# Kernel tuning notes

Measured on AMD Instinct MI355X. Metric: run time of the kernel, lower is better.

The kernel has to match this reference:

```python
import jax, jax.numpy as jnp
import numpy as np

VAR_FLOOR = 0.002
BS, A, IN, H, L, NNH, ATT, NACT = 1024, 32, 96, 64, 16, 64, 32, 16


def _lin(x, w, b):
    return x @ w.T + b


def _lrelu(x):
    return jax.nn.leaky_relu(x, 0.01)


def setup_inputs() -> dict:
    key = jax.random.key(0)
    ks = jax.random.split(key, 24)
    def w(k, o, i):
        return jax.random.normal(k, (o, i), jnp.float32) / np.float32(np.sqrt(i))
    def b(k, o):
        return jax.random.normal(k, (o,), jnp.float32) * 0.01
    N = BS * A
    return {
        "inputs": jax.random.normal(ks[0], (N, IN), jnp.float32),
        "hidden_state": jax.random.normal(ks[1], (N, H), jnp.float32),
        "eps": jax.random.normal(ks[2], (N, A * L), jnp.float32),
        "fc1_w": w(ks[3], H, IN), "fc1_b": b(ks[4], H),
        "gru_wih": w(ks[5], 3 * H, H), "gru_whh": w(ks[6], 3 * H, H),
        "gru_bih": b(ks[7], 3 * H), "gru_bhh": b(ks[8], 3 * H),
        "fc2_w": w(ks[9], NACT, H), "fc2_b": b(ks[10], NACT),
        "emb_w1": w(ks[11], NNH, H), "emb_b1": b(ks[12], NNH),
        "bn_g": jnp.ones((NNH,), jnp.float32), "bn_b": jnp.zeros((NNH,), jnp.float32),
        "emb_w2": w(ks[13], A * L * 2, NNH), "emb_b2": b(ks[14], A * L * 2),
        "msg_w1": w(ks[15], NNH, H + L), "msg_b1": b(ks[16], NNH),
        "msg_w2": w(ks[17], NACT, NNH), "msg_b2": b(ks[18], NACT),
        "wq_w": w(ks[19], ATT, H), "wq_b": b(ks[20], ATT),
        "wk_w": w(ks[21], ATT, L), "wk_b": b(ks[22], ATT),
        "bs": BS, "t": 0,
    }


def reference(inputs, hidden_state, eps, fc1_w, fc1_b, gru_wih, gru_whh, gru_bih,
              gru_bhh, fc2_w, fc2_b, emb_w1, emb_b1, bn_g, bn_b, emb_w2, emb_b2,
              msg_w1, msg_b1, msg_w2, msg_b2, wq_w, wq_b, wk_w, wk_b, bs, t):
    Hd = fc1_w.shape[0]
    x = jax.nn.relu(_lin(inputs, fc1_w, fc1_b))
    h_in = hidden_state.reshape(-1, Hd)
    # GRUCell
    gi = _lin(x, gru_wih, gru_bih)
    gh = _lin(h_in, gru_whh, gru_bhh)
    ir, iz, inn = jnp.split(gi, 3, axis=-1)
    hr, hz, hn = jnp.split(gh, 3, axis=-1)
    r = jax.nn.sigmoid(ir + hr)
    z = jax.nn.sigmoid(iz + hz)
    n = jnp.tanh(inn + r * hn)
    h = (1.0 - z) * n + z * h_in
    q = _lin(h, fc2_w, fc2_b)
    # embed_net: Linear -> BatchNorm(train) -> LeakyReLU -> Linear
    z1 = _lin(h, emb_w1, emb_b1)
    z1 = bn_g * (z1 - z1.mean(0)) / jnp.sqrt(z1.var(0) + 1e-5) + bn_b
    lat_par = _lin(_lrelu(z1), emb_w2, emb_b2)
    D = lat_par.shape[-1] // 2
    Ld = wk_w.shape[1]
    Ag = D // Ld
    mu = lat_par[:, :D]
    var = jnp.clip(jnp.exp(lat_par[:, D:]), VAR_FLOOR, None)
    latent = (mu + jnp.sqrt(var) * eps).reshape(bs, Ag, Ag, Ld)  # [b,i,j,L]
    # msg_net on (h of receiver j, latent[b,i,j])
    h3 = h.reshape(bs, Ag, Hd)
    h_rep = jnp.broadcast_to(h3[:, None, :, :], (bs, Ag, Ag, Hd))  # [b,i,j]=h[b,j]
    msg_in = jnp.concatenate([h_rep, latent], axis=-1)
    msg = _lin(_lrelu(_lin(msg_in, msg_w1, msg_b1)), msg_w2, msg_b2)  # (b,A,A,n_act)
    # attention gating
    att = wq_w.shape[0]
    query = _lin(h, wq_w, wq_b).reshape(bs, Ag, att) / np.float32(np.sqrt(att))
    key_ = _lin(latent, wk_w, wk_b)  # (b,A,A,att)
    alpha = jnp.einsum('bia,bija->bij', query, key_)
    alpha = jnp.where(jnp.eye(Ag, dtype=bool)[None], -1e9, alpha)
    alpha = jax.nn.softmax(alpha, axis=-1)
    agg = jnp.einsum('bij,bijn->bjn', alpha, msg)  # sum gated msgs over sender i
    return_q = q + agg.reshape(bs * Ag, -1)
    return (return_q, h)
```

## Files before the change

kernel.cpp:

```cpp
#include <hip/hip_runtime.h>
#include <math.h>

namespace {

constexpr int NROW = 32768;
constexpr int HDIM = 64;
constexpr int DH   = 512;

typedef __attribute__((ext_vector_type(8))) short bf16x8;
typedef __attribute__((ext_vector_type(4))) float f32x4;
typedef __attribute__((ext_vector_type(4))) unsigned uint4e;
typedef __attribute__((ext_vector_type(2))) unsigned uint2e;

__device__ __forceinline__ float sigmoidf_(float x) { return 1.f / (1.f + __expf(-x)); }
__device__ __forceinline__ float lrelu_(float x) { return x > 0.f ? x : 0.01f * x; }
__device__ __forceinline__ unsigned pkbf(float a, float b) {
  unsigned ua = __float_as_uint(a) + 0x8000u;
  unsigned ub = __float_as_uint(b) + 0x8000u;
  return __builtin_amdgcn_perm(ub, ua, 0x07060302);
}

__global__ __launch_bounds__(512, 1) void k_fgru(
    const float* __restrict__ in,
    const float* __restrict__ hprev,
    const float* __restrict__ fc1w, const float* __restrict__ fc1b,
    const float* __restrict__ wih, const float* __restrict__ whh,
    const float* __restrict__ bih, const float* __restrict__ bhh,
    float* __restrict__ hT, float* __restrict__ hout) {
  __shared__ char smem[73728];
  const int t = threadIdx.x;
  const int n0 = blockIdx.x * 128;
  short*    xS = (short*)smem;
  unsigned* gU = (unsigned*)(smem + 18432);
  float*    trF = (float*)(smem + 18432);

  const float2* wih2 = (const float2*)wih;
  const float2* whh2 = (const float2*)whh;
  {
    float2 wv[12];
#pragma unroll
    for (int i = 0; i < 12; ++i) {
      int idx = t + 512 * i;
      int row = idx >> 5, kp = idx & 31;
      wv[i] = wih2[row * 32 + kp];
    }
#pragma unroll
    for (int i = 0; i < 12; ++i) {
      int idx = t + 512 * i;
      int row = idx >> 5, kp = idx & 31;
      int gate = row >> 6, cl = row & 63;
      gU[(gate * 64 + cl) * 36 + kp] = pkbf(wv[i].x, wv[i].y);
    }
#pragma unroll
    for (int i = 0; i < 12; ++i) {
      int idx = t + 512 * i;
      int row = idx >> 5, kp = idx & 31;
      wv[i] = whh2[row * 32 + kp];
    }
#pragma unroll
    for (int i = 0; i < 12; ++i) {
      int idx = t + 512 * i;
      int row = idx >> 5, kp = idx & 31;
      int gate = row >> 6, cl = row & 63;
      gU[((gate + 3) * 64 + cl) * 36 + kp] = pkbf(wv[i].x, wv[i].y);
    }
  }

  const int w = t >> 6, l = t & 63;
  const int m = l & 15, g = l >> 4;
  const int rowA = n0 + w * 16 + m;

  bf16x8 af[3];
#pragma unroll
  for (int ks = 0; ks < 3; ++ks) {
    const float4* p = (const float4*)(in + (size_t)rowA * 96 + ks * 32 + g * 8);
    float4 a = p[0], b = p[1];
    union { unsigned u[4]; bf16x8 h; } tw;
    tw.u[0] = pkbf(a.x, a.y); tw.u[1] = pkbf(a.z, a.w);
    tw.u[2] = pkbf(b.x, b.y); tw.u[3] = pkbf(b.z, b.w);
    af[ks] = tw.h;
  }
  {
    f32x4 accx[4];
#pragma unroll
    for (int ct = 0; ct < 4; ++ct) accx[ct] = (f32x4){0.f, 0.f, 0.f, 0.f};
#pragma unroll
    for (int ct = 0; ct < 4; ++ct)
#pragma unroll
      for (int ks = 0; ks < 3; ++ks) {
        const float4* p = (const float4*)(fc1w + (ct * 16 + m) * 96 + ks * 32 + g * 8);
        float4 a = p[0], b = p[1];
        union { unsigned u[4]; bf16x8 h; } tw;
        tw.u[0] = pkbf(a.x, a.y); tw.u[1] = pkbf(a.z, a.w);
        tw.u[2] = pkbf(b.x, b.y); tw.u[3] = pkbf(b.z, b.w);
        accx[ct] = __builtin_amdgcn_mfma_f32_16x16x32_bf16(af[ks], tw.h, accx[ct], 0, 0, 0);
      }
#pragma unroll
    for (int ct = 0; ct < 4; ++ct) {
      int c = ct * 16 + m;
      float bc = fc1b[c];
#pragma unroll
      for (int reg = 0; reg < 4; ++reg) {
        int nl = w * 16 + g * 4 + reg;
        float v = fmaxf(accx[ct][reg] + bc, 0.f);
        xS[nl * 72 + c] = (short)((__float_as_uint(v) + 0x8000u) >> 16);
      }
    }
  }
  __syncthreads();

  bf16x8 ax[2], ah[2];
#pragma unroll
  for (int ks = 0; ks < 2; ++ks) {
    ax[ks] = *(const bf16x8*)(xS + (w * 16 + m) * 72 + ks * 32 + g * 8);
    const float4* p = (const float4*)(hprev + (size_t)rowA * 64 + ks * 32 + g * 8);
    float4 a = p[0], b = p[1];
    union { unsigned u[4]; bf16x8 h; } tw;
    tw.u[0] = pkbf(a.x, a.y); tw.u[1] = pkbf(a.z, a.w);
    tw.u[2] = pkbf(b.x, b.y); tw.u[3] = pkbf(b.z, b.w);
    ah[ks] = tw.h;
  }
  const short* gS = (const short*)gU;
  float hc[4][4];
#pragma unroll 1
  for (int ct = 0; ct < 4; ++ct) {
    f32x4 a_ir = (f32x4){0.f,0.f,0.f,0.f}, a_iz = (f32x4){0.f,0.f,0.f,0.f},
          a_in = (f32x4){0.f,0.f,0.f,0.f}, a_hr = (f32x4){0.f,0.f,0.f,0.f},
          a_hz = (f32x4){0.f,0.f,0.f,0.f}, a_hn = (f32x4){0.f,0.f,0.f,0.f};
    int crow = ct * 16 + m;
#pragma unroll
    for (int ks = 0; ks < 2; ++ks) {
      bf16x8 b0 = *(const bf16x8*)(gS + (0 * 64 + crow) * 72 + ks * 32 + g * 8);
      bf16x8 b1 = *(const bf16x8*)(gS + (1 * 64 + crow) * 72 + ks * 32 + g * 8);
      bf16x8 b2 = *(const bf16x8*)(gS + (2 * 64 + crow) * 72 + ks * 32 + g * 8);
      bf16x8 b3 = *(const bf16x8*)(gS + (3 * 64 + crow) * 72 + ks * 32 + g * 8);
      bf16x8 b4 = *(const bf16x8*)(gS + (4 * 64 + crow) * 72 + ks * 32 + g * 8);
      bf16x8 b5 = *(const bf16x8*)(gS + (5 * 64 + crow) * 72 + ks * 32 + g * 8);
      a_ir = __builtin_amdgcn_mfma_f32_16x16x32_bf16(ax[ks], b0, a_ir, 0, 0, 0);
      a_iz = __builtin_amdgcn_mfma_f32_16x16x32_bf16(ax[ks], b1, a_iz, 0, 0, 0);
      a_in = __builtin_amdgcn_mfma_f32_16x16x32_bf16(ax[ks], b2, a_in, 0, 0, 0);
      a_hr = __builtin_amdgcn_mfma_f32_16x16x32_bf16(ah[ks], b3, a_hr, 0, 0, 0);
      a_hz = __builtin_amdgcn_mfma_f32_16x16x32_bf16(ah[ks], b4, a_hz, 0, 0, 0);
      a_hn = __builtin_amdgcn_mfma_f32_16x16x32_bf16(ah[ks], b5, a_hn, 0, 0, 0);
    }
    float bir = bih[crow], biz = bih[64 + crow], bin = bih[128 + crow];
    float bhr = bhh[crow], bhz = bhh[64 + crow], bhn = bhh[128 + crow];
#pragma unroll
    for (int reg = 0; reg < 4; ++reg) {
      int nl = w * 16 + g * 4 + reg;
      float hv = hprev[(size_t)(n0 + nl) * 64 + crow];
      float r  = sigmoidf_(a_ir[reg] + bir + a_hr[reg] + bhr);
      float z  = sigmoidf_(a_iz[reg] + biz + a_hz[reg] + bhz);
      float nn = tanhf(a_in[reg] + bin + r * (a_hn[reg] + bhn));
      hc[ct][reg] = (1.f - z) * nn + z * hv;
    }
  }
  __syncthreads();
#pragma unroll
  for (int ct = 0; ct < 4; ++ct)
#pragma unroll
    for (int reg = 0; reg < 4; ++reg)
      trF[(ct * 16 + m) * 133 + w * 16 + g * 4 + reg] = hc[ct][reg];
  __syncthreads();
#pragma unroll
  for (int i = 0; i < 16; ++i) {
    int idx = t + 512 * i;
    int nl = idx & 127, cl = idx >> 7;
    hT[(size_t)cl * NROW + n0 + nl] = trF[cl * 133 + nl];
  }
#pragma unroll
  for (int i = 0; i < 16; ++i) {
    int idx = t + 512 * i;
    int c = idx & 63, nl = idx >> 6;
    hout[(size_t)(n0 + nl) * 64 + c] = trF[c * 133 + nl];
  }
}

__global__ __launch_bounds__(256) void k_heads(const float* __restrict__ hT,
    const float* __restrict__ fc2w, const float* __restrict__ fc2b,
    const float* __restrict__ wqw, const float* __restrict__ wkw,
    const float* __restrict__ ew1, const float* __restrict__ eb1,
    float* __restrict__ qT, float* __restrict__ qkT, float* __restrict__ z1T,
    float* __restrict__ part) {
  __shared__ char smem[36864];
  const int t = threadIdx.x;
  const int n0 = blockIdx.x * 128;
  unsigned* hU = (unsigned*)smem;
  unsigned* wU = (unsigned*)(smem + 18432);
  float* sp1 = (float*)(smem + 18432 + 13824);
  float* sp2 = sp1 + 256;
  const float qs = 0.17677669529663687f;

  {
    float va[16], vb[16];
#pragma unroll
    for (int i = 0; i < 16; ++i) {
      int idx = t + 256 * i;
      int nl = idx & 127, kp = idx >> 7;
      va[i] = hT[(size_t)(2 * kp) * NROW + n0 + nl];
      vb[i] = hT[(size_t)(2 * kp + 1) * NROW + n0 + nl];
    }
#pragma unroll
    for (int i = 0; i < 16; ++i) {
      int idx = t + 256 * i;
      int nl = idx & 127, kp = idx >> 7;
      hU[nl * 36 + kp] = pkbf(va[i], vb[i]);
    }
  }
  {
    float2 wv[10];
#pragma unroll
    for (int i = 0; i < 10; ++i) {
      int idx = t + 256 * i;
      int kp = idx & 31, cl = idx >> 5;
      const float* src = (cl < 16) ? (fc2w + cl * 64) : (ew1 + (cl - 16) * 64);
      wv[i] = *(const float2*)(src + 2 * kp);
    }
#pragma unroll
    for (int i = 0; i < 10; ++i) {
      int idx = t + 256 * i;
      int kp = idx & 31, cl = idx >> 5;
      int dst = (cl < 16) ? cl : (cl + 16);
      wU[dst * 36 + kp] = pkbf(wv[i].x, wv[i].y);
    }
  }
  {
    int kp = t & 31, ll = t >> 5;
#pragma unroll
    for (int h = 0; h < 2; ++h) {
      int row = ll + 8 * h;
      float s0 = 0.f, s1 = 0.f;
#pragma unroll
      for (int a = 0; a < 32; ++a) {
        float wk = wkw[a * 16 + row];
        s0 = fmaf(wk, wqw[a * 64 + 2 * kp], s0);
        s1 = fmaf(wk, wqw[a * 64 + 2 * kp + 1], s1);
      }
      wU[(16 + row) * 36 + kp] = pkbf(s0 * qs, s1 * qs);
    }
  }
  __syncthreads();

  const int w = t >> 6, l = t & 63;
  const int m = l & 15, g = l >> 4;
  const short* sH = (const short*)hU;
  const short* sW = (const short*)wU;

  bf16x8 af[2][2];
#pragma unroll
  for (int mt = 0; mt < 2; ++mt)
#pragma unroll
    for (int ks = 0; ks < 2; ++ks)
      af[mt][ks] = *(const bf16x8*)(sH + (w * 32 + mt * 16 + m) * 72 + ks * 32 + g * 8);

  f32x4 acc[2][6];
#pragma unroll
  for (int mt = 0; mt < 2; ++mt)
#pragma unroll
    for (int ct = 0; ct < 6; ++ct) acc[mt][ct] = (f32x4){0.f, 0.f, 0.f, 0.f};
#pragma unroll
  for (int ct = 0; ct < 6; ++ct)
#pragma unroll
    for (int ks = 0; ks < 2; ++ks) {
      bf16x8 bw = *(const bf16x8*)(sW + (ct * 16 + m) * 72 + ks * 32 + g * 8);
#pragma unroll
      for (int mt = 0; mt < 2; ++mt)
        acc[mt][ct] = __builtin_amdgcn_mfma_f32_16x16x32_bf16(af[mt][ks], bw, acc[mt][ct], 0, 0, 0);
    }

  float s1[4], s2[4];
#pragma unroll
  for (int zt = 0; zt < 4; ++zt) { s1[zt] = 0.f; s2[zt] = 0.f; }
#pragma unroll
  for (int mt = 0; mt < 2; ++mt) {
    int nb = n0 + w * 32 + mt * 16 + g * 4;
    {
      float bc = fc2b[m];
      f32x4 v;
#pragma unroll
      for (int reg = 0; reg < 4; ++reg) v[reg] = acc[mt][0][reg] + bc;
      *(f32x4*)(qT + (size_t)m * NROW + nb) = v;
    }
    *(f32x4*)(qkT + (size_t)m * NROW + nb) = acc[mt][1];
#pragma unroll
    for (int ct = 2; ct < 6; ++ct) {
      int z = (ct - 2) * 16 + m;
      float bc = eb1[z];
      f32x4 v;
#pragma unroll
      for (int reg = 0; reg < 4; ++reg) {
        float zv = acc[mt][ct][reg] + bc;
        v[reg] = zv;
        s1[ct - 2] += zv;
        s2[ct - 2] = fmaf(zv, zv, s2[ct - 2]);
      }
      *(f32x4*)(z1T + (size_t)z * NROW + nb) = v;
    }
  }
#pragma unroll
  for (int zt = 0; zt < 4; ++zt) {
    s1[zt] += __shfl_down(s1[zt], 16, 64);
    s1[zt] += __shfl_down(s1[zt], 32, 64);
    s2[zt] += __shfl_down(s2[zt], 16, 64);
    s2[zt] += __shfl_down(s2[zt], 32, 64);
  }
  if (l < 16) {
#pragma unroll
    for (int zt = 0; zt < 4; ++zt) {
      sp1[w * 64 + zt * 16 + m] = s1[zt];
      sp2[w * 64 + zt * 16 + m] = s2[zt];
    }
  }
  __syncthreads();
  if (t < 64) {
    float a1 = sp1[t] + sp1[64 + t] + sp1[128 + t] + sp1[192 + t];
    float a2 = sp2[t] + sp2[64 + t] + sp2[128 + t] + sp2[192 + t];
    part[(size_t)blockIdx.x * 128 + t] = a1;
    part[(size_t)blockIdx.x * 128 + 64 + t] = a2;
  }
}

__global__ __launch_bounds__(256) void k_bnstat(const float* __restrict__ part,
    const float* __restrict__ bng, const float* __restrict__ bnb,
    const float* __restrict__ ew2,
    float* __restrict__ stat, unsigned* __restrict__ ew2b) {
  if (blockIdx.x == 0) {
    __shared__ float red[512];
    const int t = threadIdx.x;
    const int c = t & 63, q = t >> 6;
    float s1 = 0.f, s2 = 0.f;
#pragma unroll 4
    for (int b = q; b < 256; b += 4) {
      s1 += part[(size_t)b * 128 + c];
      s2 += part[(size_t)b * 128 + 64 + c];
    }
    red[q * 64 + c] = s1;
    red[256 + q * 64 + c] = s2;
    __syncthreads();
    if (t < 64) {
      float a1 = red[t] + red[64 + t] + red[128 + t] + red[192 + t];
      float a2 = red[256 + t] + red[320 + t] + red[384 + t] + red[448 + t];
      float mean = a1 * (1.f / NROW);
      float var = a2 * (1.f / NROW) - mean * mean;
      float rstd = rsqrtf(var + 1e-5f);
      float sc = bng[t] * rstd;
      stat[t] = sc;
      stat[64 + t] = bnb[t] - mean * sc;
    }
  } else {
    const int rb = blockIdx.x - 1;
    const int t = threadIdx.x;
#pragma unroll
    for (int it = 0; it < 2; ++it) {
      int id2 = t + 256 * it;
      int r = rb * 16 + (id2 >> 5);
      int cp = id2 & 31;
      float2 v = *(const float2*)(ew2 + (size_t)r * 64 + 2 * cp);
      ew2b[(size_t)r * 32 + cp] = pkbf(v.x, v.y);
    }
  }
}

constexpr int LATB_OFF = 0;
constexpr int H3B_OFF  = 36864;
constexpr int W1H_OFF  = 41472;
constexpr int W1L_OFF  = 50688;
constexpr int W2P_OFF  = 53248;
constexpr int ALL_OFF  = 55552;
constexpr int MT_OFF   = 59776;
constexpr int QKL_OFF  = MT_OFF + 4608;
__global__ __launch_bounds__(512, 1) void k_msg(
    const unsigned* __restrict__ ew2b, const float* __restrict__ stat,
    const float* __restrict__ z1T, const float* __restrict__ eb2,
    const float* __restrict__ eps,
    const float* __restrict__ qkT,
    const float* __restrict__ qT, const float* __restrict__ hrow,
    const float* __restrict__ w1, const float* __restrict__ b1,
    const float* __restrict__ w2, const float* __restrict__ b2,
    float* __restrict__ out) {
  __shared__ char smem[80256];
  const int t = threadIdx.x;
  const int b = blockIdx.x;
  const int b32 = b * 32;
  unsigned* latB_dw = (unsigned*)(smem + LATB_OFF);

  const int w = t >> 6, l = t & 63;
  const int m = l & 15, g = l >> 4;

  {
    short* xz = (short*)(smem + MT_OFF);
    float zv[4];
#pragma unroll
    for (int it = 0; it < 4; ++it) {
      int idx = t + 512 * it;
      int i = idx & 31, c = idx >> 5;
      zv[it] = z1T[(size_t)c * NROW + b32 + i];
    }
#pragma unroll
    for (int it = 0; it < 4; ++it) {
      int idx = t + 512 * it;
      int i = idx & 31, c = idx >> 5;
      float v = lrelu_(fmaf(stat[c], zv[it], stat[64 + c]));
      xz[i * 72 + c] = (short)((__float_as_uint(v) + 0x8000u) >> 16);
    }
  }
  {
    float* qkL = (float*)(smem + QKL_OFF);
    int i = t & 31, ll = t >> 5;
    qkL[i * 20 + ll] = qkT[(size_t)ll * NROW + b32 + i];
  }
  {
    int cp = t & 31, jbase = t >> 5;
    const float2* h2 = (const float2*)hrow;
    float2 hv[2];
#pragma unroll
    for (int it = 0; it < 2; ++it)
      hv[it] = h2[((size_t)(b32 + jbase + 16 * it) * 64 + 2 * cp) >> 1];
    unsigned* dst = (unsigned*)(smem + H3B_OFF);
#pragma unroll
    for (int it = 0; it < 2; ++it)
      dst[(jbase + 16 * it) * 36 + cp] = pkbf(hv[it].x, hv[it].y);
  }
  {
    int kp = t & 31, cb = t >> 5;
    const float2* w12 = (const float2*)w1;
    float2 wv[4];
#pragma unroll
    for (int it = 0; it < 4; ++it)
      wv[it] = w12[((cb + 16 * it) * 80 + 2 * kp) >> 1];
    unsigned* dst = (unsigned*)(smem + W1H_OFF);
#pragma unroll
    for (int it = 0; it < 4; ++it)
      dst[(cb + 16 * it) * 36 + kp] = pkbf(wv[it].x, wv[it].y);
  }
  {
    int lp = t & 7, cc = t >> 3;
    const float2* w12 = (const float2*)w1;
    float2 wv = w12[(cc * 80 + 64 + 2 * lp) >> 1];
    unsigned* dst = (unsigned*)(smem + W1L_OFF);
    dst[cc * 10 + lp] = pkbf(wv.x, wv.y);
  }
  {
    int pp = t & 31, nn = t >> 5;
    const float2* w22 = (const float2*)w2;
    int p = 2 * pp;
    int c = ((p >> 2) & 3) * 16 + (p >> 4) * 4 + (p & 3);
    float2 wv0 = w22[(nn * 64 + c) >> 1];
    unsigned* dst = (unsigned*)(smem + W2P_OFF);
    dst[nn * 36 + pp] = pkbf(wv0.x, wv0.y);
  }
  __syncthreads();

  {
    const short* xzS = (const short*)(smem + MT_OFF);
    bf16x8 afz[2][2];
#pragma unroll
    for (int mt = 0; mt < 2; ++mt)
#pragma unroll
      for (int ks = 0; ks < 2; ++ks)
        afz[mt][ks] = *(const bf16x8*)(xzS + (mt * 16 + m) * 72 + ks * 32 + g * 8);
    const uint4e* w4 = (const uint4e*)ew2b;
    const float stdfloor = 0.04472135955f;
#pragma unroll 2
    for (int ci8 = 0; ci8 < 4; ++ci8) {
      int ci = w * 4 + ci8;
      int c = ci * 16 + m;
      union { uint4e u; bf16x8 h; } bmu[2], blv[2];
#pragma unroll
      for (int ks = 0; ks < 2; ++ks) {
        bmu[ks].u = w4[(size_t)(ci * 16 + m) * 8 + ks * 4 + g];
        blv[ks].u = w4[(size_t)(512 + ci * 16 + m) * 8 + ks * 4 + g];
      }
      float ep[2][4];
#pragma unroll
      for (int mt = 0; mt < 2; ++mt)
#pragma unroll
        for (int reg = 0; reg < 4; ++reg)
          ep[mt][reg] = eps[(size_t)(b32 + mt * 16 + g * 4 + reg) * 512 + c];
      f32x4 accm[2], accl[2];
#pragma unroll
      for (int mt = 0; mt < 2; ++mt) {
        accm[mt] = (f32x4){0.f, 0.f, 0.f, 0.f};
        accl[mt] = (f32x4){0.f, 0.f, 0.f, 0.f};
      }
#pragma unroll
      for (int ks = 0; ks < 2; ++ks)
#pragma unroll
        for (int mt = 0; mt < 2; ++mt) {
          accm[mt] = __builtin_amdgcn_mfma_f32_16x16x32_bf16(afz[mt][ks], bmu[ks].h, accm[mt], 0, 0, 0);
          accl[mt] = __builtin_amdgcn_mfma_f32_16x16x32_bf16(afz[mt][ks], blv[ks].h, accl[mt], 0, 0, 0);
        }
      float ebm = eb2[c], ebl = eb2[DH + c];
#pragma unroll
      for (int mt = 0; mt < 2; ++mt)
#pragma unroll
        for (int reg = 0; reg < 4; ++reg) {
          float mu = accm[mt][reg] + ebm;
          float lv = accl[mt][reg] + ebl;
          float sd = fmaxf(__expf(0.5f * lv), stdfloor);
          float lat = fmaf(sd, ep[mt][reg], mu);
          float lat2 = __shfl_xor(lat, 1, 64);
          if (!(m & 1)) {
            int i = mt * 16 + g * 4 + reg;
            latB_dw[(i * 32 + ci) * 9 + (m >> 1)] = pkbf(lat, lat2);
          }
        }
    }
  }
  __syncthreads();

  {
    const float* qkL = (const float*)(smem + QKL_OFF);
    float* alL = (float*)(smem + ALL_OFF);
#pragma unroll 1
    for (int p = 0; p < 2; ++p) {
      int i = (t >> 5) + 16 * p;
      int j = t & 31;
      const unsigned* lr = latB_dw + (i * 32 + j) * 9;
      float acc = 0.f;
#pragma unroll
      for (int d = 0; d < 8; ++d) {
        unsigned u = lr[d];
        float lo = __uint_as_float(u << 16);
        float hi = __uint_as_float(u & 0xffff0000u);
        acc = fmaf(lo, qkL[i * 20 + 2 * d], acc);
        acc = fmaf(hi, qkL[i * 20 + 2 * d + 1], acc);
      }
      if (j == i) acc = -1e9f;
      float mx = acc;
#pragma unroll
      for (int msk = 16; msk > 0; msk >>= 1) mx = fmaxf(mx, __shfl_xor(mx, msk, 32));
      float e = __expf(acc - mx);
      float s = e;
#pragma unroll
      for (int msk = 16; msk > 0; msk >>= 1) s += __shfl_xor(s, msk, 32);
      alL[i * 33 + j] = e / s;
    }
  }

  const int n15 = l & 15, q = l >> 4;
  const int jh = w & 1, ibase = (w >> 1) * 8;
  const bool kact = (q < 2);

  f32x4 hp[4];
#pragma unroll
  for (int ct = 0; ct < 4; ++ct) hp[ct] = (f32x4){0.f, 0.f, 0.f, 0.f};
#pragma unroll
  for (int ct = 0; ct < 4; ++ct)
#pragma unroll
    for (int ks = 0; ks < 2; ++ks) {
      bf16x8 aF = *(const bf16x8*)(smem + W1H_OFF + (ct * 16 + n15) * 144 + ks * 64 + q * 16);
      bf16x8 bF = *(const bf16x8*)(smem + H3B_OFF + (jh * 16 + n15) * 144 + ks * 64 + q * 16);
      hp[ct] = __builtin_amdgcn_mfma_f32_16x16x32_bf16(aF, bF, hp[ct], 0, 0, 0);
    }
#pragma unroll
  for (int ct = 0; ct < 4; ++ct)
#pragma unroll
    for (int reg = 0; reg < 4; ++reg)
      hp[ct][reg] += b1[ct * 16 + q * 4 + reg];

  bf16x8 aL[4];
#pragma unroll
  for (int ct = 0; ct < 4; ++ct) {
    union { unsigned u[4]; bf16x8 h; } tmp;
    tmp.u[0] = tmp.u[1] = tmp.u[2] = tmp.u[3] = 0u;
    if (kact) {
      const unsigned* p = (const unsigned*)(smem + W1L_OFF) + (ct * 16 + n15) * 10 + q * 4;
      uint2e d0 = *(const uint2e*)p;
      uint2e d1 = *(const uint2e*)(p + 2);
      tmp.u[0] = d0.x; tmp.u[1] = d0.y; tmp.u[2] = d1.x; tmp.u[3] = d1.y;
    }
    aL[ct] = tmp.h;
  }
  bf16x8 w2F[2];
#pragma unroll
  for (int ks = 0; ks < 2; ++ks)
    w2F[ks] = *(const bf16x8*)(smem + W2P_OFF + n15 * 144 + ks * 64 + q * 16);
  float b2v[4];
#pragma unroll
  for (int reg = 0; reg < 4; ++reg) b2v[reg] = b2[q * 4 + reg];

  __syncthreads();

  float agg[4] = {0.f, 0.f, 0.f, 0.f};
  char* wb = smem + MT_OFF + w * 2560;
  const float* alLf = (const float*)(smem + ALL_OFF);
#pragma unroll 1
  for (int it = 0; it < 8; ++it) {
    int ii = ibase + it;
    int r = ii * 32 + jh * 16 + n15;
    union { unsigned u[4]; bf16x8 h; } latF;
    latF.u[0] = latF.u[1] = latF.u[2] = latF.u[3] = 0u;
    if (kact) {
      const unsigned* p = latB_dw + r * 9 + q * 4;
      latF.u[0] = p[0]; latF.u[1] = p[1]; latF.u[2] = p[2]; latF.u[3] = p[3];
    }
    f32x4 acc[4];
#pragma unroll
    for (int ct = 0; ct < 4; ++ct) {
      acc[ct] = (f32x4){0.f, 0.f, 0.f, 0.f};
      acc[ct] = __builtin_amdgcn_mfma_f32_16x16x32_bf16(aL[ct], latF.h, acc[ct], 0, 0, 0);
    }
#pragma unroll
    for (int h = 0; h < 2; ++h) {
      float m0[4], m1[4];
#pragma unroll
      for (int reg = 0; reg < 4; ++reg) {
        float v0 = acc[2 * h][reg] + hp[2 * h][reg];
        float v1 = acc[2 * h + 1][reg] + hp[2 * h + 1][reg];
        m0[reg] = fmaxf(v0, 0.01f * v0);
        m1[reg] = fmaxf(v1, 0.01f * v1);
      }
      uint4e pk4;
      pk4.x = pkbf(m0[0], m0[1]); pk4.y = pkbf(m0[2], m0[3]);
      pk4.z = pkbf(m1[0], m1[1]); pk4.w = pkbf(m1[2], m1[3]);
      int qp = (2 * q + h) & 3;
      *(uint4e*)(wb + (q >> 1) * 1280 + n15 * 80 + qp * 16) = pk4;
    }
    f32x4 msg = (f32x4){0.f, 0.f, 0.f, 0.f};
#pragma unroll
    for (int ks = 0; ks < 2; ++ks) {
      bf16x8 mF = *(const bf16x8*)(wb + ks * 1280 + n15 * 80 + q * 16);
      msg = __builtin_amdgcn_mfma_f32_16x16x32_bf16(w2F[ks], mF, msg, 0, 0, 0);
    }
    float aw = alLf[ii * 33 + jh * 16 + n15];
#pragma unroll
    for (int reg = 0; reg < 4; ++reg)
      agg[reg] = fmaf(aw, msg[reg] + b2v[reg], agg[reg]);
  }
  {
    f32x4 av; av[0] = agg[0]; av[1] = agg[1]; av[2] = agg[2]; av[3] = agg[3];
    *(f32x4*)(wb + n15 * 80 + q * 16) = av;
  }
  __syncthreads();
  {
    int jg = t >> 4, nn = t & 15;
    int jh2 = jg >> 4, jl = jg & 15;
    float s = qT[(size_t)nn * NROW + b32 + jg];
#pragma unroll
    for (int k = 0; k < 4; ++k)
      s += *(const float*)(smem + MT_OFF + (jh2 + 2 * k) * 2560 + jl * 80 + nn * 4);
    out[(size_t)b * 512 + t] = s;
  }
}

}

extern "C" void kernel_launch(void* const* d_in, const int* in_sizes, int n_in,
                              void* d_out, int out_size, void* d_ws, size_t ws_size,
                              hipStream_t stream) {
  (void)in_sizes; (void)n_in; (void)out_size; (void)ws_size;
  const float* inputs = (const float*)d_in[0];
  const float* hidden = (const float*)d_in[1];
  const float* eps    = (const float*)d_in[2];
  const float* fc1w   = (const float*)d_in[3];
  const float* fc1b   = (const float*)d_in[4];
  const float* wih    = (const float*)d_in[5];
  const float* whh    = (const float*)d_in[6];
  const float* bih    = (const float*)d_in[7];
  const float* bhh    = (const float*)d_in[8];
  const float* fc2w   = (const float*)d_in[9];
  const float* fc2b   = (const float*)d_in[10];
  const float* ew1    = (const float*)d_in[11];
  const float* eb1    = (const float*)d_in[12];
  const float* bng    = (const float*)d_in[13];
  const float* bnb    = (const float*)d_in[14];
  const float* ew2    = (const float*)d_in[15];
  const float* eb2    = (const float*)d_in[16];
  const float* w1     = (const float*)d_in[17];
  const float* b1     = (const float*)d_in[18];
  const float* w2     = (const float*)d_in[19];
  const float* b2     = (const float*)d_in[20];
  const float* wqw    = (const float*)d_in[21];
  const float* wkw    = (const float*)d_in[23];

  float* ws = (float*)d_ws;
  float* hT     = ws;
  float* qT     = ws + 2097152;
  float* qkT    = ws + 2621440;
  float* z1T    = ws + 3670016;
  float* part   = ws + 5767168;
  float* stat   = ws + 5832704;
  unsigned* ew2b = (unsigned*)(ws + 5832832);

  float* out_q = (float*)d_out;
  float* out_h = (float*)d_out + 524288;

  hipLaunchKernelGGL(k_fgru, dim3(256), dim3(512), 0, stream,
                     inputs, hidden, fc1w, fc1b, wih, whh, bih, bhh, hT, out_h);
  hipLaunchKernelGGL(k_heads, dim3(256), dim3(256), 0, stream,
                     hT, fc2w, fc2b, wqw, wkw, ew1, eb1, qT, qkT, z1T, part);
  hipLaunchKernelGGL(k_bnstat, dim3(65), dim3(256), 0, stream, part, bng, bnb, ew2, stat, ew2b);
  hipLaunchKernelGGL(k_msg, dim3(1024), dim3(512), 0, stream,
                     ew2b, stat, z1T, eb2, eps, qkT, qT, out_h, w1, b1, w2, b2, out_q);
}
```

Baseline: 227.4 us.

## Fuse heads projection kernel into GRU kernel, dropping transposed h buffer

Merges the fc2/query-key/embedding-layer-1 projections into the GRU kernel. The new hidden state goes to LDS as bf16 and feeds MFMA directly, with per-block BN partial sums computed in the same kernel. This removes one kernel launch, plus the global write and re-read of the transposed hidden state hT. In exchange, the GRU kernel uses more LDS (about 90KB) and more registers, and it loads the extra weights in every block.

```diff
diff --git a/kernel.cpp b/kernel.cpp
--- a/kernel.cpp
+++ b/kernel.cpp
@@ -26,13 +26,21 @@
     const float* __restrict__ fc1w, const float* __restrict__ fc1b,
     const float* __restrict__ wih, const float* __restrict__ whh,
     const float* __restrict__ bih, const float* __restrict__ bhh,
-    float* __restrict__ hT, float* __restrict__ hout) {
-  __shared__ char smem[73728];
+    const float* __restrict__ fc2w, const float* __restrict__ fc2b,
+    const float* __restrict__ wqw, const float* __restrict__ wkw,
+    const float* __restrict__ ew1, const float* __restrict__ eb1,
+    float* __restrict__ qT, float* __restrict__ qkT, float* __restrict__ z1T,
+    float* __restrict__ part, float* __restrict__ hout) {
+  __shared__ char smem[91648];
   const int t = threadIdx.x;
   const int n0 = blockIdx.x * 128;
   short*    xS = (short*)smem;
   unsigned* gU = (unsigned*)(smem + 18432);
   float*    trF = (float*)(smem + 18432);
+  unsigned* wU = (unsigned*)(smem + 73728);
+  float*    sp1 = (float*)(smem + 87552);
+  float*    sp2 = (float*)(smem + 89600);
+  const float qs = 0.17677669529663687f;
 
   const float2* wih2 = (const float2*)wih;
   const float2* whh2 = (const float2*)whh;
@@ -64,6 +72,34 @@
       int gate = row >> 6, cl = row & 63;
       gU[((gate + 3) * 64 + cl) * 36 + kp] = pkbf(wv[i].x, wv[i].y);
     }
+  }
+  {
+    float2 wv[5];
+#pragma unroll
+    for (int i = 0; i < 5; ++i) {
+      int idx = t + 512 * i;
+      int kp = idx & 31, cl = idx >> 5;
+      const float* src = (cl < 16) ? (fc2w + cl * 64) : (ew1 + (cl - 16) * 64);
+      wv[i] = *(const float2*)(src + 2 * kp);
+    }
+#pragma unroll
+    for (int i = 0; i < 5; ++i) {
+      int idx = t + 512 * i;
+      int kp = idx & 31, cl = idx >> 5;
+      int dst = (cl < 16) ? cl : (cl + 16);
+      wU[dst * 36 + kp] = pkbf(wv[i].x, wv[i].y);
+    }
+  }
+  {
+    int kp = t & 31, row = t >> 5;
+    float s0 = 0.f, s1 = 0.f;
+#pragma unroll
+    for (int a = 0; a < 32; ++a) {
+      float wk = wkw[a * 16 + row];
+      s0 = fmaf(wk, wqw[a * 64 + 2 * kp], s0);
+      s1 = fmaf(wk, wqw[a * 64 + 2 * kp + 1], s1);
+    }
+    wU[(16 + row) * 36 + kp] = pkbf(s0 * qs, s1 * qs);
   }
 
   const int w = t >> 6, l = t & 63;
@@ -155,6 +191,31 @@
       hc[ct][reg] = (1.f - z) * nn + z * hv;
     }
   }
+#pragma unroll
+  for (int ct = 0; ct < 4; ++ct)
+#pragma unroll
+    for (int reg = 0; reg < 4; ++reg) {
+      int nl = w * 16 + g * 4 + reg;
+      xS[nl * 72 + ct * 16 + m] =
+          (short)((__float_as_uint(hc[ct][reg]) + 0x8000u) >> 16);
+    }
+
+  bf16x8 af2[2];
+#pragma unroll
+  for (int ks = 0; ks < 2; ++ks)
+    af2[ks] = *(const bf16x8*)(xS + (w * 16 + m) * 72 + ks * 32 + g * 8);
+  const short* sW = (const short*)wU;
+  f32x4 acc[6];
+#pragma unroll
+  for (int ct = 0; ct < 6; ++ct) acc[ct] = (f32x4){0.f, 0.f, 0.f, 0.f};
+#pragma unroll
+  for (int ct = 0; ct < 6; ++ct)
+#pragma unroll
+    for (int ks = 0; ks < 2; ++ks) {
+      bf16x8 bw = *(const bf16x8*)(sW + (ct * 16 + m) * 72 + ks * 32 + g * 8);
+      acc[ct] = __builtin_amdgcn_mfma_f32_16x16x32_bf16(af2[ks], bw, acc[ct], 0, 0, 0);
+    }
+
   __syncthreads();
 #pragma unroll
   for (int ct = 0; ct < 4; ++ct)
@@ -162,126 +223,26 @@
     for (int reg = 0; reg < 4; ++reg)
       trF[(ct * 16 + m) * 133 + w * 16 + g * 4 + reg] = hc[ct][reg];
   __syncthreads();
-#pragma unroll
-  for (int i = 0; i < 16; ++i) {
-    int idx = t + 512 * i;
-    int nl = idx & 127, cl = idx >> 7;
-    hT[(size_t)cl * NROW + n0 + nl] = trF[cl * 133 + nl];
-  }
 #pragma unroll
   for (int i = 0; i < 16; ++i) {
     int idx = t + 512 * i;
     int c = idx & 63, nl = idx >> 6;
     hout[(size_t)(n0 + nl) * 64 + c] = trF[c * 133 + nl];
   }
-}
-
-__global__ __launch_bounds__(256) void k_heads(const float* __restrict__ hT,
-    const float* __restrict__ fc2w, const float* __restrict__ fc2b,
-    const float* __restrict__ wqw, const float* __restrict__ wkw,
-    const float* __restrict__ ew1, const float* __restrict__ eb1,
-    float* __restrict__ qT, float* __restrict__ qkT, float* __restrict__ z1T,
-    float* __restrict__ part) {
-  __shared__ char smem[36864];
-  const int t = threadIdx.x;
-  const int n0 = blockIdx.x * 128;
-  unsigned* hU = (unsigned*)smem;
-  unsigned* wU = (unsigned*)(smem + 18432);
-  float* sp1 = (float*)(smem + 18432 + 13824);
-  float* sp2 = sp1 + 256;
-  const float qs = 0.17677669529663687f;
-
-  {
-    float va[16], vb[16];
-#pragma unroll
-    for (int i = 0; i < 16; ++i) {
-      int idx = t + 256 * i;
-      int nl = idx & 127, kp = idx >> 7;
-      va[i] = hT[(size_t)(2 * kp) * NROW + n0 + nl];
-      vb[i] = hT[(size_t)(2 * kp + 1) * NROW + n0 + nl];
-    }
-#pragma unroll
-    for (int i = 0; i < 16; ++i) {
-      int idx = t + 256 * i;
-      int nl = idx & 127, kp = idx >> 7;
-      hU[nl * 36 + kp] = pkbf(va[i], vb[i]);
-    }
-  }
-  {
-    float2 wv[10];
-#pragma unroll
-    for (int i = 0; i < 10; ++i) {
-      int idx = t + 256 * i;
-      int kp = idx & 31, cl = idx >> 5;
-      const float* src = (cl < 16) ? (fc2w + cl * 64) : (ew1 + (cl - 16) * 64);
-      wv[i] = *(const float2*)(src + 2 * kp);
-    }
-#pragma unroll
-    for (int i = 0; i < 10; ++i) {
-      int idx = t + 256 * i;
-      int kp = idx & 31, cl = idx >> 5;
-      int dst = (cl < 16) ? cl : (cl + 16);
-      wU[dst * 36 + kp] = pkbf(wv[i].x, wv[i].y);
-    }
-  }
-  {
-    int kp = t & 31, ll = t >> 5;
-#pragma unroll
-    for (int h = 0; h < 2; ++h) {
-      int row = ll + 8 * h;
-      float s0 = 0.f, s1 = 0.f;
-#pragma unroll
-      for (int a = 0; a < 32; ++a) {
-        float wk = wkw[a * 16 + row];
-        s0 = fmaf(wk, wqw[a * 64 + 2 * kp], s0);
-        s1 = fmaf(wk, wqw[a * 64 + 2 * kp + 1], s1);
-      }
-      wU[(16 + row) * 36 + kp] = pkbf(s0 * qs, s1 * qs);
-    }
-  }
-  __syncthreads();
-
-  const int w = t >> 6, l = t & 63;
-  const int m = l & 15, g = l >> 4;
-  const short* sH = (const short*)hU;
-  const short* sW = (const short*)wU;
-
-  bf16x8 af[2][2];
-#pragma unroll
-  for (int mt = 0; mt < 2; ++mt)
-#pragma unroll
-    for (int ks = 0; ks < 2; ++ks)
-      af[mt][ks] = *(const bf16x8*)(sH + (w * 32 + mt * 16 + m) * 72 + ks * 32 + g * 8);
-
-  f32x4 acc[2][6];
-#pragma unroll
-  for (int mt = 0; mt < 2; ++mt)
-#pragma unroll
-    for (int ct = 0; ct < 6; ++ct) acc[mt][ct] = (f32x4){0.f, 0.f, 0.f, 0.f};
-#pragma unroll
-  for (int ct = 0; ct < 6; ++ct)
-#pragma unroll
-    for (int ks = 0; ks < 2; ++ks) {
-      bf16x8 bw = *(const bf16x8*)(sW + (ct * 16 + m) * 72 + ks * 32 + g * 8);
-#pragma unroll
-      for (int mt = 0; mt < 2; ++mt)
-        acc[mt][ct] = __builtin_amdgcn_mfma_f32_16x16x32_bf16(af[mt][ks], bw, acc[mt][ct], 0, 0, 0);
-    }
 
   float s1[4], s2[4];
 #pragma unroll
   for (int zt = 0; zt < 4; ++zt) { s1[zt] = 0.f; s2[zt] = 0.f; }
-#pragma unroll
-  for (int mt = 0; mt < 2; ++mt) {
-    int nb = n0 + w * 32 + mt * 16 + g * 4;
+  {
+    int nb = n0 + w * 16 + g * 4;
     {
       float bc = fc2b[m];
       f32x4 v;
 #pragma unroll
-      for (int reg = 0; reg < 4; ++reg) v[reg] = acc[mt][0][reg] + bc;
+      for (int reg = 0; reg < 4; ++reg) v[reg] = acc[0][reg] + bc;
       *(f32x4*)(qT + (size_t)m * NROW + nb) = v;
     }
-    *(f32x4*)(qkT + (size_t)m * NROW + nb) = acc[mt][1];
+    *(f32x4*)(qkT + (size_t)m * NROW + nb) = acc[1];
 #pragma unroll
     for (int ct = 2; ct < 6; ++ct) {
       int z = (ct - 2) * 16 + m;
@@ -289,7 +250,7 @@
       f32x4 v;
 #pragma unroll
       for (int reg = 0; reg < 4; ++reg) {
-        float zv = acc[mt][ct][reg] + bc;
+        float zv = acc[ct][reg] + bc;
         v[reg] = zv;
         s1[ct - 2] += zv;
         s2[ct - 2] = fmaf(zv, zv, s2[ct - 2]);
@@ -313,8 +274,12 @@
   }
   __syncthreads();
   if (t < 64) {
-    float a1 = sp1[t] + sp1[64 + t] + sp1[128 + t] + sp1[192 + t];
-    float a2 = sp2[t] + sp2[64 + t] + sp2[128 + t] + sp2[192 + t];
+    float a1 = 0.f, a2 = 0.f;
+#pragma unroll
+    for (int k = 0; k < 8; ++k) {
+      a1 += sp1[k * 64 + t];
+      a2 += sp2[k * 64 + t];
+    }
     part[(size_t)blockIdx.x * 128 + t] = a1;
     part[(size_t)blockIdx.x * 128 + 64 + t] = a2;
   }
@@ -675,7 +640,6 @@
   const float* wkw    = (const float*)d_in[23];
 
   float* ws = (float*)d_ws;
-  float* hT     = ws;
   float* qT     = ws + 2097152;
   float* qkT    = ws + 2621440;
   float* z1T    = ws + 3670016;
@@ -687,9 +651,9 @@
   float* out_h = (float*)d_out + 524288;
 
   hipLaunchKernelGGL(k_fgru, dim3(256), dim3(512), 0, stream,
-                     inputs, hidden, fc1w, fc1b, wih, whh, bih, bhh, hT, out_h);
-  hipLaunchKernelGGL(k_heads, dim3(256), dim3(256), 0, stream,
-                     hT, fc2w, fc2b, wqw, wkw, ew1, eb1, qT, qkT, z1T, part);
+                     inputs, hidden, fc1w, fc1b, wih, whh, bih, bhh,
+                     fc2w, fc2b, wqw, wkw, ew1, eb1,
+                     qT, qkT, z1T, part, out_h);
   hipLaunchKernelGGL(k_bnstat, dim3(65), dim3(256), 0, stream, part, bng, bnb, ew2, stat, ew2b);
   hipLaunchKernelGGL(k_msg, dim3(1024), dim3(512), 0, stream,
                      ew2b, stat, z1T, eb2, eps, qkT, qT, out_h, w1, b1, w2, b2, out_q);
```

Result: faster. 211.8 us (-6.9%).
